# Kernel optimization log

Hardware: AMD Instinct MI355X
Metric: run time of the kernel (lower is better)

## Reference

```python
import jax, jax.numpy as jnp
import numpy as np

HEAD_DIM = 256
N_Q = 8
N_KV = 4
HIDDEN = 2304
WINDOW = 1024
SOFT_CAP = 50.0
MAX_WAVELENGTH = 10000.0


def _rope(x, start_index=0):
    # x: [b, s, n, h]. keras_hub RotaryEmbedding (rotate-half convention),
    # followed by Gemma's interleave permutation of the feature dim.
    b, s, n, h = x.shape
    inv_freq = 1.0 / (MAX_WAVELENGTH ** (jnp.arange(0, h, 2, dtype=jnp.float32) / h))
    pos = jnp.arange(s, dtype=jnp.float32) + start_index
    freq = pos[:, None] * inv_freq[None, :]            # [s, h/2]
    emb = jnp.concatenate([freq, freq], axis=-1)[None, :, None, :]  # [1, s, 1, h]
    cos, sin = jnp.cos(emb).astype(x.dtype), jnp.sin(emb).astype(x.dtype)
    x1, x2 = jnp.split(x, 2, axis=-1)
    rot = jnp.concatenate([-x2, x1], axis=-1)
    y = x * cos + rot * sin
    # Gemma _apply_rope: split halves then interleave (same permutation on q and k)
    a, b2 = jnp.split(y, 2, axis=-1)
    return jnp.stack([a, b2], axis=-1).reshape(x.shape)


def setup_inputs() -> dict:
    key = jax.random.key(0)
    ks = jax.random.split(key, 5)
    B, T, D = 2, 2048, HIDDEN
    x = jax.random.normal(ks[0], (B, T, D), dtype=jnp.float32)
    # causal mask [b, q_len, kv_len]
    causal = jnp.tril(jnp.ones((T, T), dtype=bool))
    attention_mask = jnp.broadcast_to(causal[None], (B, T, T))
    scale = 0.02
    Wq = jax.random.normal(ks[1], (N_Q, D, HEAD_DIM), dtype=jnp.float32) * scale
    Wk = jax.random.normal(ks[2], (N_KV, D, HEAD_DIM), dtype=jnp.float32) * scale
    Wv = jax.random.normal(ks[3], (N_KV, D, HEAD_DIM), dtype=jnp.float32) * scale
    Wo = jax.random.normal(ks[4], (N_Q, HEAD_DIM, D), dtype=jnp.float32) * scale
    return {"x": x, "attention_mask": attention_mask, "Wq": Wq, "Wk": Wk, "Wv": Wv, "Wo": Wo}


def reference(x, attention_mask, Wq, Wk, Wv, Wo):
    b, t, d = x.shape
    q = jnp.einsum('btd,ndh->btnh', x, Wq)
    k = jnp.einsum('bsd,kdh->bskh', x, Wk)
    v = jnp.einsum('bsd,kdh->bskh', x, Wv)
    q = _rope(q)
    k = _rope(k)
    s = k.shape[1]
    # sliding window band mask (triu(-w+1) & tril(w-1)), rows sliced at cache_update_index=0
    i = jnp.arange(s)[:, None]
    j = jnp.arange(s)[None, :]
    sliding = (j - i <= WINDOW - 1) & (i - j <= WINDOW - 1)
    mask = attention_mask & sliding[None, :t, :s]      # [b, t, s]
    q = q * jnp.asarray(1.0 / np.sqrt(HEAD_DIM), dtype=q.dtype)
    g = N_Q // N_KV
    qg = q.reshape(b, t, N_KV, g, HEAD_DIM)
    logits = jnp.einsum('btkgh,bskh->bkgts', qg, k).astype(jnp.float32)
    logits = jnp.tanh(logits / SOFT_CAP) * SOFT_CAP    # logit soft-cap
    m = mask[:, None, None, :, :]                      # [b, 1, 1, t, s]
    logits = jnp.where(m, logits, jnp.float32(-1e30))
    probs = jax.nn.softmax(logits, axis=-1).astype(q.dtype)
    out = jnp.einsum('bkgts,bskh->btkgh', probs, v).reshape(b, t, N_Q, HEAD_DIM)
    no_attended = jnp.all(~attention_mask, axis=-1, keepdims=True)[..., None]  # [b, t, 1, 1]
    out = jnp.where(no_attended, jnp.zeros_like(out), out)
    return jnp.einsum('btnh,nhd->btd', out, Wo)
```

## Files before the change

kernel.cpp:

```cpp
#include <hip/hip_runtime.h>
#include <math.h>

#define HEAD_DIM 256
#define N_Q 8
#define N_KV 4
#define HIDDEN 2304
#define WINDOW 1024
#define BATCH 2
#define SEQ 2048
#define BT (BATCH*SEQ)

typedef unsigned short u16;
typedef __attribute__((ext_vector_type(8))) short bf16x8;
typedef __attribute__((ext_vector_type(4))) float f32x4;

__device__ __forceinline__ u16 f2bf(float f) {
    union { float f; unsigned u; } c; c.f = f;
    unsigned r = c.u + 0x7FFF + ((c.u >> 16) & 1);
    return (u16)(r >> 16);
}
__device__ __forceinline__ float bf2f(u16 b) {
    union { float f; unsigned u; } c; c.u = ((unsigned)b) << 16;
    return c.f;
}

__global__ __launch_bounds__(256) void convert_x_kernel(
    const float* __restrict__ x, u16* __restrict__ xb, int n8)
{
    int i = blockIdx.x * 256 + threadIdx.x;
    if (i >= n8) return;
    const float4 a = ((const float4*)x)[2*i];
    const float4 b = ((const float4*)x)[2*i+1];
    u16 o[8] = { f2bf(a.x), f2bf(a.y), f2bf(a.z), f2bf(a.w),
                 f2bf(b.x), f2bf(b.y), f2bf(b.z), f2bf(b.w) };
    ((uint4*)xb)[i] = *(const uint4*)o;
}

__global__ __launch_bounds__(256) void wqkv_t_kernel(
    const float* __restrict__ Wq, const float* __restrict__ Wk,
    const float* __restrict__ Wv, u16* __restrict__ Wt)
{
    __shared__ float t[64][65];
    const int j = blockIdx.z;
    const float* W = (j < 8)  ? Wq + (size_t)j*HIDDEN*HEAD_DIM
                   : (j < 12) ? Wk + (size_t)(j-8)*HIDDEN*HEAD_DIM
                              : Wv + (size_t)(j-12)*HIDDEN*HEAD_DIM;
    const int d0 = blockIdx.x * 64, h0 = blockIdx.y * 64;
    const int tid = threadIdx.x;
    {
        const int r = tid >> 4, c4 = tid & 15;
        #pragma unroll
        for (int rr = r; rr < 64; rr += 16) {
            const float4 v = *(const float4*)(W + (size_t)(d0+rr)*HEAD_DIM + h0 + c4*4);
            t[rr][c4*4+0] = v.x; t[rr][c4*4+1] = v.y;
            t[rr][c4*4+2] = v.z; t[rr][c4*4+3] = v.w;
        }
    }
    __syncthreads();
    {
        const int hh = tid >> 2;
        #pragma unroll
        for (int it = 0; it < 2; it++) {
            const int chunk = (tid & 3) + it*4;
            u16 tmp[8];
            #pragma unroll
            for (int jj = 0; jj < 8; jj++) tmp[jj] = f2bf(t[chunk*8+jj][hh]);
            *(uint4*)&Wt[(size_t)(j*256 + h0 + hh)*HIDDEN + d0 + chunk*8] = *(const uint4*)tmp;
        }
    }
}

__global__ __launch_bounds__(256) void wo_t_kernel(
    const float* __restrict__ Wo, u16* __restrict__ Wot)
{
    __shared__ float t[64][65];
    const int k0 = blockIdx.x * 64, d0 = blockIdx.y * 64;
    const int tid = threadIdx.x;
    {
        const int r = tid >> 4, c4 = tid & 15;
        #pragma unroll
        for (int rr = r; rr < 64; rr += 16) {
            const float4 v = *(const float4*)(Wo + (size_t)(k0+rr)*HIDDEN + d0 + c4*4);
            t[rr][c4*4+0] = v.x; t[rr][c4*4+1] = v.y;
            t[rr][c4*4+2] = v.z; t[rr][c4*4+3] = v.w;
        }
    }
    __syncthreads();
    {
        const int dd = tid >> 2;
        #pragma unroll
        for (int it = 0; it < 2; it++) {
            const int chunk = (tid & 3) + it*4;
            u16 tmp[8];
            #pragma unroll
            for (int jj = 0; jj < 8; jj++) tmp[jj] = f2bf(t[chunk*8+jj][dd]);
            *(uint4*)&Wot[(size_t)(d0 + dd)*(N_Q*HEAD_DIM) + k0 + chunk*8] = *(const uint4*)tmp;
        }
    }
}

template<int KK>
__device__ __forceinline__ void g256_ld_b(const u16 (&BsB)[16384], bf16x8 (&bf)[4],
                                          int wcol, int l16, int quad, int axor)
{
    #pragma unroll
    for (int j = 0; j < 4; j++)
        bf[j] = *(const bf16x8*)(&BsB[(wcol*64 + j*16 + l16)*64 + (((KK<<2)|quad)^axor)*8]);
}
template<int MH, int KK>
__device__ __forceinline__ void g256_ld_a(const u16 (&AsB)[16384], bf16x8 (&af)[4],
                                          int wrow, int l16, int quad, int axor)
{
    #pragma unroll
    for (int i = 0; i < 4; i++)
        af[i] = *(const bf16x8*)(&AsB[(wrow*128 + MH*64 + i*16 + l16)*64 + (((KK<<2)|quad)^axor)*8]);
}
template<int MH>
__device__ __forceinline__ void g256_mfma(const bf16x8 (&af)[4], const bf16x8 (&bf)[4],
                                          f32x4 (&acc)[8][4])
{
    __builtin_amdgcn_s_setprio(1);
    #pragma unroll
    for (int i = 0; i < 4; i++)
        #pragma unroll
        for (int j = 0; j < 4; j++)
            acc[MH*4+i][j] = __builtin_amdgcn_mfma_f32_16x16x32_bf16(
                                 af[i], bf[j], acc[MH*4+i][j], 0, 0, 0);
    __builtin_amdgcn_s_setprio(0);
}

#define STG256(DST, SRCP, R0, KT)                                              \
    __builtin_amdgcn_global_load_lds(                                          \
        (const __attribute__((address_space(1))) unsigned int*)                \
            ((SRCP) + (size_t)(R0)*K + (size_t)(KT)*64),                       \
        (__attribute__((address_space(3))) unsigned int*)                      \
            (&DST[((R0) + wave*8)*64]),                                        \
        16, 0, 0)

#define WAITV(N) asm volatile("s_waitcnt vmcnt(" #N ")" ::: "memory")
#define BAR()    __builtin_amdgcn_s_barrier()

template<typename OutT>
__global__ __launch_bounds__(512, 2) void gemm256_kernel(
    const u16* __restrict__ A, const u16* __restrict__ Bt,
    OutT* __restrict__ C, int M, int N, int K)
{
    __shared__ __align__(16) u16 As0[16384];
    __shared__ __align__(16) u16 As1[16384];
    __shared__ __align__(16) u16 Bs0[16384];
    __shared__ __align__(16) u16 Bs1[16384];

    const int nwg = gridDim.x;
    const int bid = blockIdx.x;
    const int cpx = nwg >> 3;
    const int swz = (bid & 7) * cpx + (bid >> 3);
    const int NX  = N >> 8;
    const int m0  = (swz / NX) << 8;
    const int n0  = (swz % NX) << 8;

    const int tid  = threadIdx.x;
    const int lane = tid & 63;
    const int wave = tid >> 6;
    const int wrow = wave >> 2;
    const int wcol = wave & 3;
    const int l16  = lane & 15;
    const int quad = lane >> 4;
    const int axor = l16 & 7;

    const int srow8  = lane >> 3;
    const int schunk = (lane & 7) ^ srow8;
    const u16* Ag = A  + (size_t)(m0 + wave*8 + srow8)*K + schunk*8;
    const u16* Bg = Bt + (size_t)(n0 + wave*8 + srow8)*K + schunk*8;

    f32x4 acc[8][4];
    #pragma unroll
    for (int i = 0; i < 8; i++)
        #pragma unroll
        for (int j = 0; j < 4; j++) acc[i][j] = (f32x4){0.f,0.f,0.f,0.f};
    bf16x8 af[4], bf[4];

    STG256(Bs0, Bg,   0, 0); STG256(Bs0, Bg,  64, 0);
    STG256(Bs0, Bg, 128, 0); STG256(Bs0, Bg, 192, 0);
    STG256(As0, Ag,   0, 0); STG256(As0, Ag, 128, 0);
    STG256(As0, Ag,  64, 0); STG256(As0, Ag, 192, 0);
    STG256(Bs1, Bg,   0, 1); STG256(Bs1, Bg,  64, 1);
    WAITV(4);
    BAR();

    const int NT2 = K >> 7;
    for (int t = 0; t < NT2; ++t) {
        const int T1 = 2*t+1, T2 = 2*t+2, T3 = 2*t+3;
        const bool nl = (t < NT2-1);

        g256_ld_b<0>(Bs0, bf, wcol, l16, quad, axor);
        g256_ld_a<0,0>(As0, af, wrow, l16, quad, axor);
        STG256(Bs1, Bg, 128, T1); STG256(Bs1, Bg, 192, T1);
        BAR();
        g256_mfma<0>(af, bf, acc);
        WAITV(4);
        BAR();

        g256_ld_a<1,0>(As0, af, wrow, l16, quad, axor);
        STG256(As1, Ag, 0, T1); STG256(As1, Ag, 128, T1);
        BAR();
        g256_mfma<1>(af, bf, acc);
        BAR();

        g256_ld_b<1>(Bs0, bf, wcol, l16, quad, axor);
        g256_ld_a<0,1>(As0, af, wrow, l16, quad, axor);
        STG256(As1, Ag, 64, T1); STG256(As1, Ag, 192, T1);
        BAR();
        g256_mfma<0>(af, bf, acc);
        BAR();

        g256_ld_a<1,1>(As0, af, wrow, l16, quad, axor);
        if (nl) { STG256(Bs0, Bg, 0, T2); STG256(Bs0, Bg, 64, T2); }
        BAR();
        g256_mfma<1>(af, bf, acc);
        if (nl) { WAITV(4); }
        else    { WAITV(0); }
        BAR();

        g256_ld_b<0>(Bs1, bf, wcol, l16, quad, axor);
        g256_ld_a<0,0>(As1, af, wrow, l16, quad, axor);
        if (nl) { STG256(Bs0, Bg, 128, T2); STG256(Bs0, Bg, 192, T2); }
        BAR();
        g256_mfma<0>(af, bf, acc);
        WAITV(4);
        BAR();

        g256_ld_a<1,0>(As1, af, wrow, l16, quad, axor);
        if (nl) { STG256(As0, Ag, 0, T2); STG256(As0, Ag, 128, T2); }
        BAR();
        g256_mfma<1>(af, bf, acc);
        BAR();

        g256_ld_b<1>(Bs1, bf, wcol, l16, quad, axor);
        g256_ld_a<0,1>(As1, af, wrow, l16, quad, axor);
        if (nl) { STG256(As0, Ag, 64, T2); STG256(As0, Ag, 192, T2); }
        BAR();
        g256_mfma<0>(af, bf, acc);
        BAR();

        g256_ld_a<1,1>(As1, af, wrow, l16, quad, axor);
        if (nl) { STG256(Bs1, Bg, 0, T3); STG256(Bs1, Bg, 64, T3); }
        BAR();
        g256_mfma<1>(af, bf, acc);
        WAITV(4);
        BAR();
    }

    #pragma unroll
    for (int ii = 0; ii < 8; ii++) {
        const int rbase = m0 + wrow*128 + ii*16 + quad*4;
        #pragma unroll
        for (int j = 0; j < 4; j++) {
            const int col = n0 + wcol*64 + j*16 + l16;
            #pragma unroll
            for (int r = 0; r < 4; r++) {
                const float v = acc[ii][j][r];
                if constexpr (sizeof(OutT) == 2)
                    ((u16*)C)[(size_t)(rbase + r)*N + col] = f2bf(v);
                else
                    ((float*)C)[(size_t)(rbase + r)*N + col] = v;
            }
        }
    }
}

__global__ __launch_bounds__(256) void rope_kernel(
    const u16* __restrict__ raw, u16* __restrict__ qb, u16* __restrict__ kbf)
{
    const int r   = blockIdx.x;
    const int pos = r & (SEQ-1);
    const int tid = threadIdx.x;
    const u16* row = raw + (size_t)r * 4096;
    const float LOG1E4 = 9.210340371976184f;

    #pragma unroll
    for (int p = tid; p < 1024; p += 256) {
        const int n = p >> 7, j = p & 127;
        const float lo = bf2f(row[n*256 + j]);
        const float hi = bf2f(row[n*256 + j + 128]);
        const float inv = __expf(-LOG1E4 * (float)j * (1.0f/128.0f));
        float s, c; sincosf((float)pos * inv, &s, &c);
        qb[((size_t)r*N_Q + n)*HEAD_DIM + j]       = f2bf((lo*c - hi*s) * 0.0625f);
        qb[((size_t)r*N_Q + n)*HEAD_DIM + j + 128] = f2bf((hi*c + lo*s) * 0.0625f);
    }
    #pragma unroll
    for (int p = tid; p < 512; p += 256) {
        const int n = p >> 7, j = p & 127;
        const float lo = bf2f(row[2048 + n*256 + j]);
        const float hi = bf2f(row[2048 + n*256 + j + 128]);
        const float inv = __expf(-LOG1E4 * (float)j * (1.0f/128.0f));
        float s, c; sincosf((float)pos * inv, &s, &c);
        kbf[((size_t)r*N_KV + n)*HEAD_DIM + j]       = f2bf(lo*c - hi*s);
        kbf[((size_t)r*N_KV + n)*HEAD_DIM + j + 128] = f2bf(hi*c + lo*s);
    }
}

__global__ __launch_bounds__(256) void vtrans_kernel(
    const u16* __restrict__ raw, u16* __restrict__ vtt)
{
    __shared__ u16 T[32*264];
    const int blk = blockIdx.x;
    const int sc  = blk & 63;
    const int bk  = blk >> 6;
    const int b   = bk >> 2, kh = bk & 3;
    const int tid = threadIdx.x;

    const u16* rrow = raw + (size_t)(b*SEQ + sc*32)*4096 + 3072 + kh*256;
    {
        const int s = tid >> 3;
        #pragma unroll
        for (int it = 0; it < 4; it++) {
            const int seg = (tid & 7) + it*8;
            *(uint4*)&T[s*264 + seg*8] = *(const uint4*)(rrow + (size_t)s*4096 + seg*8);
        }
    }
    __syncthreads();
    u16* out = vtt + (size_t)blk*8192;
    #pragma unroll
    for (int it = 0; it < 4; it++) {
        const int o = tid + it*256;
        const int h = o >> 2, ss = o & 3;
        u16 tmp[8];
        #pragma unroll
        for (int j = 0; j < 8; j++) tmp[j] = T[(ss*8 + j)*264 + h];
        *(uint4*)(out + h*32 + ((ss ^ (h & 3))*8)) = *(const uint4*)tmp;
    }
}

#define AQT 64
__global__ __launch_bounds__(256) void attn_mfma_kernel(
    const u16* __restrict__ qb, const u16* __restrict__ kb,
    const u16* __restrict__ vtt, u16* __restrict__ ao)
{
    __shared__ u16 Ks[32*264];
    __shared__ u16 Vs[256*32];
    __shared__ u16 Ps[64*40];
    __shared__ float lsum[64];

    const int qh = blockIdx.y;
    const int kh = qh >> 1;
    const int bx = ((blockIdx.y >> 2) & 1) ? (gridDim.x - 1 - (int)blockIdx.x)
                                           : (int)blockIdx.x;
    const int t0 = bx * AQT;
    const int b  = t0 >> 11;
    const int tb = t0 & (SEQ-1);
    const int tid  = threadIdx.x;
    const int wave = tid >> 6;
    const int lane = tid & 63;
    const int l16  = lane & 15;
    const int quad = lane >> 4;

    bf16x8 qf[8];
    {
        const u16* qrow = qb + ((size_t)(t0 + wave*16 + l16)*N_Q + qh)*HEAD_DIM + quad*8;
        #pragma unroll
        for (int c = 0; c < 8; c++) qf[c] = *(const bf16x8*)(qrow + c*32);
    }

    f32x4 o[4][4];
    #pragma unroll
    for (int i = 0; i < 4; i++)
        #pragma unroll
        for (int j = 0; j < 4; j++) o[i][j] = (f32x4){0.f,0.f,0.f,0.f};
    float lpart[4] = {0.f, 0.f, 0.f, 0.f};

    int s_begin = tb - (WINDOW-1); if (s_begin < 0) s_begin = 0;
    const int st0 = s_begin & ~31;

    const u16* kbase = kb  + ((size_t)(b*SEQ)*N_KV + kh)*HEAD_DIM;
    const u16* vbase = vtt + ((size_t)(b*N_KV + kh)*SEQ)*HEAD_DIM;

    for (int st = st0; st < tb + AQT; st += 32) {
        __syncthreads();
        {
            const u16* vtile = vbase + (size_t)st*HEAD_DIM;
            #pragma unroll
            for (int c = 0; c < 4; c++) {
                const int off = wave*2048 + c*512;
                __builtin_amdgcn_global_load_lds(
                    (const __attribute__((address_space(1))) unsigned int*)(vtile + off + lane*8),
                    (__attribute__((address_space(3))) unsigned int*)&Vs[off],
                    16, 0, 0);
            }
            const int s = tid >> 3;
            const u16* krow = kbase + (size_t)(st + s)*(N_KV*HEAD_DIM);
            #pragma unroll
            for (int it = 0; it < 4; it++) {
                const int seg = (tid & 7) + it*8;
                *(uint4*)&Ks[s*264 + seg*8] = *(const uint4*)(krow + seg*8);
            }
        }
        __syncthreads();

        f32x4 sc[2];
        #pragma unroll
        for (int sf = 0; sf < 2; sf++) {
            f32x4 a = (f32x4){0.f,0.f,0.f,0.f};
            const u16* kr = &Ks[(sf*16 + l16)*264 + quad*8];
            #pragma unroll
            for (int c = 0; c < 8; c++)
                a = __builtin_amdgcn_mfma_f32_16x16x32_bf16(
                        qf[c], *(const bf16x8*)(kr + c*32), a, 0, 0, 0);
            sc[sf] = a;
        }

        #pragma unroll
        for (int sf = 0; sf < 2; sf++) {
            const int sg = st + sf*16 + l16;
            #pragma unroll
            for (int r = 0; r < 4; r++) {
                const int tg = tb + wave*16 + quad*4 + r;
                const float e1 = __expf(sc[sf][r] * 0.04f);
                float p = __expf(-100.0f / (e1 + 1.0f));
                const bool ok = (sg <= tg) && (tg - sg < WINDOW);
                p = ok ? p : 0.0f;
                lpart[r] += p;
                Ps[(wave*16 + quad*4 + r)*40 + sf*16 + l16] = f2bf(p);
            }
        }
        __syncthreads();

        bf16x8 ap[4];
        #pragma unroll
        for (int i = 0; i < 4; i++)
            ap[i] = *(const bf16x8*)&Ps[(i*16 + l16)*40 + quad*8];
        #pragma unroll
        for (int j = 0; j < 4; j++) {
            const int hr = wave*64 + j*16 + l16;
            const bf16x8 bv = *(const bf16x8*)&Vs[hr*32 + ((quad ^ (l16 & 3))*8)];
            #pragma unroll
            for (int i = 0; i < 4; i++)
                o[i][j] = __builtin_amdgcn_mfma_f32_16x16x32_bf16(ap[i], bv, o[i][j], 0, 0, 0);
        }
    }

    #pragma unroll
    for (int r = 0; r < 4; r++) {
        float s = lpart[r];
        #pragma unroll
        for (int sh = 1; sh <= 8; sh <<= 1) s += __shfl_xor(s, sh, 64);
        if (l16 == 0) lsum[wave*16 + quad*4 + r] = s;
    }
    __syncthreads();

    #pragma unroll
    for (int i = 0; i < 4; i++) {
        #pragma unroll
        for (int r = 0; r < 4; r++) {
            const int rl  = i*16 + quad*4 + r;
            const float inv = 1.0f / (lsum[rl] + 1e-30f);
            u16* arow = ao + ((size_t)(t0 + rl)*N_Q + qh)*HEAD_DIM + wave*64 + l16;
            #pragma unroll
            for (int j = 0; j < 4; j++)
                arow[j*16] = f2bf(o[i][j][r] * inv);
        }
    }
}

extern "C" void kernel_launch(void* const* d_in, const int* in_sizes, int n_in,
                              void* d_out, int out_size, void* d_ws, size_t ws_size,
                              hipStream_t stream)
{
    const float* x  = (const float*)d_in[0];
    const float* Wq = (const float*)d_in[2];
    const float* Wk = (const float*)d_in[3];
    const float* Wv = (const float*)d_in[4];
    const float* Wo = (const float*)d_in[5];
    float* out = (float*)d_out;

    char* w = (char*)d_ws;
    u16* qbuf = (u16*)(w);
    u16* kbuf = (u16*)(w +  16777216ull);
    u16* vtt  = (u16*)(w +  25165824ull);
    u16* aob  = (u16*)(w +  33554432ull);
    u16* xb   = (u16*)(w +  50331648ull);
    u16* wt1  = (u16*)(w +  69206016ull);
    u16* wot  = (u16*)(w +  88080384ull);
    u16* raw  = (u16*)(w +  97517568ull);

    const int n8 = BT*HIDDEN/8;
    convert_x_kernel<<<(n8+255)/256, 256, 0, stream>>>(x, xb, n8);
    wqkv_t_kernel<<<dim3(HIDDEN/64, HEAD_DIM/64, 16), 256, 0, stream>>>(Wq, Wk, Wv, wt1);
    wo_t_kernel<<<dim3(N_Q*HEAD_DIM/64, HIDDEN/64), 256, 0, stream>>>(Wo, wot);

    gemm256_kernel<u16><<<(BT/256)*(4096/256), 512, 0, stream>>>(
        xb, wt1, raw, BT, 4096, HIDDEN);
    rope_kernel<<<BT, 256, 0, stream>>>(raw, qbuf, kbuf);
    vtrans_kernel<<<BATCH*N_KV*64, 256, 0, stream>>>(raw, vtt);
    attn_mfma_kernel<<<dim3(BT/AQT, N_Q), 256, 0, stream>>>(qbuf, kbuf, vtt, aob);
    gemm256_kernel<float><<<(BT/256)*(HIDDEN/256), 512, 0, stream>>>(
        aob, wot, out, BT, HIDDEN, N_Q*HEAD_DIM);
}
```

Before: 372.7 us.

## Restructure GEMM to 4-stage BK=32 LDS pipeline with double-buffered fragments

Reworks the 256x256 GEMM main loop from two BK=64 LDS buffers to four BK=32 stages, with a matching swizzle and a new global-to-LDS load mapping. It double-buffers the A and B register fragments (X/Y) so fragment reads for the next MFMA group overlap the current one, and adds sched_barriers to pin the ordering. The aim is deeper prefetch and better hiding of load latency under the MFMAs. In exchange it executes more barriers per unit of K, and fragment double-buffering raises register pressure under launch_bounds(512,2).

Result: slower. 386.3 us (+3.7%).

```diff
diff --git a/kernel.cpp b/kernel.cpp
--- a/kernel.cpp
+++ b/kernel.cpp
@@ -99,25 +99,23 @@
     }
 }
 
-template<int KK>
-__device__ __forceinline__ void g256_ld_b(const u16 (&BsB)[16384], bf16x8 (&bf)[4],
-                                          int wcol, int l16, int quad, int axor)
+__device__ __forceinline__ void ldA4(const u16 (&B)[8192], bf16x8 (&s)[4],
+                                     int base, int MH)
+{
+    #pragma unroll
+    for (int i = 0; i < 4; i++)
+        s[i] = *(const bf16x8*)&B[base + MH*2048 + i*512];
+}
+__device__ __forceinline__ void ldB4(const u16 (&B)[8192], bf16x8 (&s)[4],
+                                     int base)
 {
     #pragma unroll
     for (int j = 0; j < 4; j++)
-        bf[j] = *(const bf16x8*)(&BsB[(wcol*64 + j*16 + l16)*64 + (((KK<<2)|quad)^axor)*8]);
-}
-template<int MH, int KK>
-__device__ __forceinline__ void g256_ld_a(const u16 (&AsB)[16384], bf16x8 (&af)[4],
-                                          int wrow, int l16, int quad, int axor)
-{
-    #pragma unroll
-    for (int i = 0; i < 4; i++)
-        af[i] = *(const bf16x8*)(&AsB[(wrow*128 + MH*64 + i*16 + l16)*64 + (((KK<<2)|quad)^axor)*8]);
+        s[j] = *(const bf16x8*)&B[base + j*512];
 }
 template<int MH>
-__device__ __forceinline__ void g256_mfma(const bf16x8 (&af)[4], const bf16x8 (&bf)[4],
-                                          f32x4 (&acc)[8][4])
+__device__ __forceinline__ void mfma16(const bf16x8 (&af)[4], const bf16x8 (&bf)[4],
+                                       f32x4 (&acc)[8][4])
 {
     __builtin_amdgcn_s_setprio(1);
     #pragma unroll
@@ -129,26 +127,32 @@
     __builtin_amdgcn_s_setprio(0);
 }
 
-#define STG256(DST, SRCP, R0, KT)                                              \
+#define WAITV(N) asm volatile("s_waitcnt vmcnt(" #N ")" ::: "memory")
+#define BAR()    __builtin_amdgcn_s_barrier()
+#define SCHEDB() __builtin_amdgcn_sched_barrier(0)
+
+#define STG(DST, SRCP, R0, KT)                                                 \
     __builtin_amdgcn_global_load_lds(                                          \
         (const __attribute__((address_space(1))) unsigned int*)                \
-            ((SRCP) + (size_t)(R0)*K + (size_t)(KT)*64),                       \
+            ((SRCP) + (size_t)(R0)*K + (size_t)(KT)*32),                       \
         (__attribute__((address_space(3))) unsigned int*)                      \
-            (&DST[((R0) + wave*8)*64]),                                        \
+            (&DST[((R0) + wave*16)*32]),                                       \
         16, 0, 0)
-
-#define WAITV(N) asm volatile("s_waitcnt vmcnt(" #N ")" ::: "memory")
-#define BAR()    __builtin_amdgcn_s_barrier()
+#define STG2(DST, SRCP, KT) do { STG(DST, SRCP, 0, KT); STG(DST, SRCP, 128, KT); } while(0)
 
 template<typename OutT>
 __global__ __launch_bounds__(512, 2) void gemm256_kernel(
     const u16* __restrict__ A, const u16* __restrict__ Bt,
     OutT* __restrict__ C, int M, int N, int K)
 {
-    __shared__ __align__(16) u16 As0[16384];
-    __shared__ __align__(16) u16 As1[16384];
-    __shared__ __align__(16) u16 Bs0[16384];
-    __shared__ __align__(16) u16 Bs1[16384];
+    __shared__ __align__(16) u16 As0[8192];
+    __shared__ __align__(16) u16 As1[8192];
+    __shared__ __align__(16) u16 As2[8192];
+    __shared__ __align__(16) u16 As3[8192];
+    __shared__ __align__(16) u16 Bs0[8192];
+    __shared__ __align__(16) u16 Bs1[8192];
+    __shared__ __align__(16) u16 Bs2[8192];
+    __shared__ __align__(16) u16 Bs3[8192];
 
     const int nwg = gridDim.x;
     const int bid = blockIdx.x;
@@ -165,89 +169,116 @@
     const int wcol = wave & 3;
     const int l16  = lane & 15;
     const int quad = lane >> 4;
-    const int axor = l16 & 7;
-
-    const int srow8  = lane >> 3;
-    const int schunk = (lane & 7) ^ srow8;
-    const u16* Ag = A  + (size_t)(m0 + wave*8 + srow8)*K + schunk*8;
-    const u16* Bg = Bt + (size_t)(n0 + wave*8 + srow8)*K + schunk*8;
+
+    const int srow4  = lane >> 2;
+    const int schunk = (lane & 3) ^ (srow4 & 3);
+    const u16* Ag = A  + (size_t)(m0 + wave*16 + srow4)*K + schunk*8;
+    const u16* Bg = Bt + (size_t)(n0 + wave*16 + srow4)*K + schunk*8;
+
+    const int quad2 = quad ^ (l16 & 3);
+    const int aBase = (wrow*128 + l16)*32 + quad2*8;
+    const int bBase = (wcol*64  + l16)*32 + quad2*8;
 
     f32x4 acc[8][4];
     #pragma unroll
     for (int i = 0; i < 8; i++)
         #pragma unroll
         for (int j = 0; j < 4; j++) acc[i][j] = (f32x4){0.f,0.f,0.f,0.f};
-    bf16x8 af[4], bf[4];
-
-    STG256(Bs0, Bg,   0, 0); STG256(Bs0, Bg,  64, 0);
-    STG256(Bs0, Bg, 128, 0); STG256(Bs0, Bg, 192, 0);
-    STG256(As0, Ag,   0, 0); STG256(As0, Ag, 128, 0);
-    STG256(As0, Ag,  64, 0); STG256(As0, Ag, 192, 0);
-    STG256(Bs1, Bg,   0, 1); STG256(Bs1, Bg,  64, 1);
-    WAITV(4);
+    bf16x8 afX[4], afY[4], bfX[4], bfY[4];
+
+    STG2(Bs0, Bg, 0); STG2(As0, Ag, 0);
+    STG2(Bs1, Bg, 1); STG2(As1, Ag, 1);
+    STG2(Bs2, Bg, 2); STG2(As2, Ag, 2);
+    WAITV(8);
     BAR();
-
-    const int NT2 = K >> 7;
-    for (int t = 0; t < NT2; ++t) {
-        const int T1 = 2*t+1, T2 = 2*t+2, T3 = 2*t+3;
-        const bool nl = (t < NT2-1);
-
-        g256_ld_b<0>(Bs0, bf, wcol, l16, quad, axor);
-        g256_ld_a<0,0>(As0, af, wrow, l16, quad, axor);
-        STG256(Bs1, Bg, 128, T1); STG256(Bs1, Bg, 192, T1);
-        BAR();
-        g256_mfma<0>(af, bf, acc);
-        WAITV(4);
-        BAR();
-
-        g256_ld_a<1,0>(As0, af, wrow, l16, quad, axor);
-        STG256(As1, Ag, 0, T1); STG256(As1, Ag, 128, T1);
-        BAR();
-        g256_mfma<1>(af, bf, acc);
-        BAR();
-
-        g256_ld_b<1>(Bs0, bf, wcol, l16, quad, axor);
-        g256_ld_a<0,1>(As0, af, wrow, l16, quad, axor);
-        STG256(As1, Ag, 64, T1); STG256(As1, Ag, 192, T1);
-        BAR();
-        g256_mfma<0>(af, bf, acc);
-        BAR();
-
-        g256_ld_a<1,1>(As0, af, wrow, l16, quad, axor);
-        if (nl) { STG256(Bs0, Bg, 0, T2); STG256(Bs0, Bg, 64, T2); }
-        BAR();
-        g256_mfma<1>(af, bf, acc);
-        if (nl) { WAITV(4); }
-        else    { WAITV(0); }
-        BAR();
-
-        g256_ld_b<0>(Bs1, bf, wcol, l16, quad, axor);
-        g256_ld_a<0,0>(As1, af, wrow, l16, quad, axor);
-        if (nl) { STG256(Bs0, Bg, 128, T2); STG256(Bs0, Bg, 192, T2); }
-        BAR();
-        g256_mfma<0>(af, bf, acc);
-        WAITV(4);
-        BAR();
-
-        g256_ld_a<1,0>(As1, af, wrow, l16, quad, axor);
-        if (nl) { STG256(As0, Ag, 0, T2); STG256(As0, Ag, 128, T2); }
-        BAR();
-        g256_mfma<1>(af, bf, acc);
-        BAR();
-
-        g256_ld_b<1>(Bs1, bf, wcol, l16, quad, axor);
-        g256_ld_a<0,1>(As1, af, wrow, l16, quad, axor);
-        if (nl) { STG256(As0, Ag, 64, T2); STG256(As0, Ag, 192, T2); }
-        BAR();
-        g256_mfma<0>(af, bf, acc);
-        BAR();
-
-        g256_ld_a<1,1>(As1, af, wrow, l16, quad, axor);
-        if (nl) { STG256(Bs1, Bg, 0, T3); STG256(Bs1, Bg, 64, T3); }
-        BAR();
-        g256_mfma<1>(af, bf, acc);
-        WAITV(4);
-        BAR();
+    ldB4(Bs0, bfX, bBase);
+    ldA4(As0, afX, aBase, 0);
+
+    const int NT = K >> 5;
+
+    for (int t = 0; t < NT-4; t += 4) {
+        ldA4(As0, afY, aBase, 1);
+        STG2(Bs3, Bg, t+3);
+        WAITV(6); SCHEDB(); BAR();
+        mfma16<0>(afX, bfX, acc);
+        BAR();
+        ldB4(Bs1, bfY, bBase);
+        ldA4(As1, afX, aBase, 0);
+        STG2(As3, Ag, t+3);
+        SCHEDB(); BAR();
+        mfma16<1>(afY, bfX, acc);
+        BAR();
+        ldA4(As1, afY, aBase, 1);
+        STG2(Bs0, Bg, t+4);
+        WAITV(6); SCHEDB(); BAR();
+        mfma16<0>(afX, bfY, acc);
+        BAR();
+        ldB4(Bs2, bfX, bBase);
+        ldA4(As2, afX, aBase, 0);
+        STG2(As0, Ag, t+4);
+        SCHEDB(); BAR();
+        mfma16<1>(afY, bfY, acc);
+        BAR();
+        ldA4(As2, afY, aBase, 1);
+        STG2(Bs1, Bg, t+5);
+        WAITV(6); SCHEDB(); BAR();
+        mfma16<0>(afX, bfX, acc);
+        BAR();
+        ldB4(Bs3, bfY, bBase);
+        ldA4(As3, afX, aBase, 0);
+        STG2(As1, Ag, t+5);
+        SCHEDB(); BAR();
+        mfma16<1>(afY, bfX, acc);
+        BAR();
+        ldA4(As3, afY, aBase, 1);
+        STG2(Bs2, Bg, t+6);
+        WAITV(6); SCHEDB(); BAR();
+        mfma16<0>(afX, bfY, acc);
+        BAR();
+        ldB4(Bs0, bfX, bBase);
+        ldA4(As0, afX, aBase, 0);
+        STG2(As2, Ag, t+6);
+        SCHEDB(); BAR();
+        mfma16<1>(afY, bfY, acc);
+        BAR();
+    }
+
+    {
+        const int t = NT-4;
+        ldA4(As0, afY, aBase, 1);
+        STG2(Bs3, Bg, t+3);
+        WAITV(6); SCHEDB(); BAR();
+        mfma16<0>(afX, bfX, acc);
+        BAR();
+        ldB4(Bs1, bfY, bBase);
+        ldA4(As1, afX, aBase, 0);
+        STG2(As3, Ag, t+3);
+        SCHEDB(); BAR();
+        mfma16<1>(afY, bfX, acc);
+        BAR();
+        ldA4(As1, afY, aBase, 1);
+        WAITV(4); SCHEDB(); BAR();
+        mfma16<0>(afX, bfY, acc);
+        BAR();
+        ldB4(Bs2, bfX, bBase);
+        ldA4(As2, afX, aBase, 0);
+        SCHEDB(); BAR();
+        mfma16<1>(afY, bfY, acc);
+        BAR();
+        ldA4(As2, afY, aBase, 1);
+        WAITV(0); SCHEDB(); BAR();
+        mfma16<0>(afX, bfX, acc);
+        BAR();
+        ldB4(Bs3, bfY, bBase);
+        ldA4(As3, afX, aBase, 0);
+        SCHEDB(); BAR();
+        mfma16<1>(afY, bfX, acc);
+        BAR();
+        ldA4(As3, afY, aBase, 1);
+        SCHEDB(); BAR();
+        mfma16<0>(afX, bfY, acc);
+        BAR();
+        mfma16<1>(afY, bfY, acc);
     }
 
     #pragma unroll
@@ -267,6 +298,9 @@
         }
     }
 }
+
+#undef STG2
+#undef STG
 
 __global__ __launch_bounds__(256) void rope_kernel(
     const u16* __restrict__ raw, u16* __restrict__ qb, u16* __restrict__ kbf)
```

## Double-buffer GEMM fragment registers to overlap LDS reads with MFMA

Applied to the files above, without the earlier changes.

Splits the A/B fragment registers into two sets (X/Y) so the LDS read for the next sub-step is issued before the MFMA batch of the current one, giving a one-stage software pipeline with a peeled prologue and epilogue. Adds sched_barrier fences and loosens the vmcnt waits so global-to-LDS loads stay in flight longer. The aim is to hide LDS read latency behind matrix work. In exchange it uses more VGPRs under the 512-thread, 2-block launch bound, which may cause spills, and it relies on subtle correctness of barrier and wait placement.

After: 386.1 us. 3.6% more time.

```diff
diff --git a/kernel.cpp b/kernel.cpp
--- a/kernel.cpp
+++ b/kernel.cpp
@@ -139,6 +139,7 @@
 
 #define WAITV(N) asm volatile("s_waitcnt vmcnt(" #N ")" ::: "memory")
 #define BAR()    __builtin_amdgcn_s_barrier()
+#define SCHEDB() __builtin_amdgcn_sched_barrier(0)
 
 template<typename OutT>
 __global__ __launch_bounds__(512, 2) void gemm256_kernel(
@@ -177,77 +178,119 @@
     for (int i = 0; i < 8; i++)
         #pragma unroll
         for (int j = 0; j < 4; j++) acc[i][j] = (f32x4){0.f,0.f,0.f,0.f};
-    bf16x8 af[4], bf[4];
+    bf16x8 afX[4], afY[4], bfX[4], bfY[4];
 
     STG256(Bs0, Bg,   0, 0); STG256(Bs0, Bg,  64, 0);
     STG256(Bs0, Bg, 128, 0); STG256(Bs0, Bg, 192, 0);
     STG256(As0, Ag,   0, 0); STG256(As0, Ag, 128, 0);
     STG256(As0, Ag,  64, 0); STG256(As0, Ag, 192, 0);
     STG256(Bs1, Bg,   0, 1); STG256(Bs1, Bg,  64, 1);
-    WAITV(4);
+    WAITV(2);
     BAR();
+    g256_ld_b<0>(Bs0, bfX, wcol, l16, quad, axor);
+    g256_ld_a<0,0>(As0, afX, wrow, l16, quad, axor);
 
     const int NT2 = K >> 7;
-    for (int t = 0; t < NT2; ++t) {
+
+    for (int t = 0; t < NT2-1; ++t) {
         const int T1 = 2*t+1, T2 = 2*t+2, T3 = 2*t+3;
-        const bool nl = (t < NT2-1);
-
-        g256_ld_b<0>(Bs0, bf, wcol, l16, quad, axor);
-        g256_ld_a<0,0>(As0, af, wrow, l16, quad, axor);
+
+        g256_ld_a<1,0>(As0, afY, wrow, l16, quad, axor);
         STG256(Bs1, Bg, 128, T1); STG256(Bs1, Bg, 192, T1);
-        BAR();
-        g256_mfma<0>(af, bf, acc);
-        WAITV(4);
-        BAR();
-
-        g256_ld_a<1,0>(As0, af, wrow, l16, quad, axor);
+        SCHEDB(); BAR();
+        g256_mfma<0>(afX, bfX, acc);
+        BAR();
+
+        g256_ld_b<1>(Bs0, bfY, wcol, l16, quad, axor);
+        g256_ld_a<0,1>(As0, afX, wrow, l16, quad, axor);
         STG256(As1, Ag, 0, T1); STG256(As1, Ag, 128, T1);
-        BAR();
-        g256_mfma<1>(af, bf, acc);
-        BAR();
-
-        g256_ld_b<1>(Bs0, bf, wcol, l16, quad, axor);
-        g256_ld_a<0,1>(As0, af, wrow, l16, quad, axor);
+        SCHEDB(); BAR();
+        g256_mfma<1>(afY, bfX, acc);
+        BAR();
+
+        g256_ld_a<1,1>(As0, afY, wrow, l16, quad, axor);
         STG256(As1, Ag, 64, T1); STG256(As1, Ag, 192, T1);
-        BAR();
-        g256_mfma<0>(af, bf, acc);
-        BAR();
-
-        g256_ld_a<1,1>(As0, af, wrow, l16, quad, axor);
-        if (nl) { STG256(Bs0, Bg, 0, T2); STG256(Bs0, Bg, 64, T2); }
-        BAR();
-        g256_mfma<1>(af, bf, acc);
-        if (nl) { WAITV(4); }
-        else    { WAITV(0); }
-        BAR();
-
-        g256_ld_b<0>(Bs1, bf, wcol, l16, quad, axor);
-        g256_ld_a<0,0>(As1, af, wrow, l16, quad, axor);
-        if (nl) { STG256(Bs0, Bg, 128, T2); STG256(Bs0, Bg, 192, T2); }
-        BAR();
-        g256_mfma<0>(af, bf, acc);
-        WAITV(4);
-        BAR();
-
-        g256_ld_a<1,0>(As1, af, wrow, l16, quad, axor);
-        if (nl) { STG256(As0, Ag, 0, T2); STG256(As0, Ag, 128, T2); }
-        BAR();
-        g256_mfma<1>(af, bf, acc);
-        BAR();
-
-        g256_ld_b<1>(Bs1, bf, wcol, l16, quad, axor);
-        g256_ld_a<0,1>(As1, af, wrow, l16, quad, axor);
-        if (nl) { STG256(As0, Ag, 64, T2); STG256(As0, Ag, 192, T2); }
-        BAR();
-        g256_mfma<0>(af, bf, acc);
-        BAR();
-
-        g256_ld_a<1,1>(As1, af, wrow, l16, quad, axor);
-        if (nl) { STG256(Bs1, Bg, 0, T3); STG256(Bs1, Bg, 64, T3); }
-        BAR();
-        g256_mfma<1>(af, bf, acc);
-        WAITV(4);
-        BAR();
+        SCHEDB(); BAR();
+        g256_mfma<0>(afX, bfY, acc);
+        WAITV(2);
+        BAR();
+
+        g256_ld_b<0>(Bs1, bfX, wcol, l16, quad, axor);
+        g256_ld_a<0,0>(As1, afX, wrow, l16, quad, axor);
+        STG256(Bs0, Bg, 0, T2); STG256(Bs0, Bg, 64, T2);
+        SCHEDB(); BAR();
+        g256_mfma<1>(afY, bfY, acc);
+        WAITV(2);
+        BAR();
+
+        g256_ld_a<1,0>(As1, afY, wrow, l16, quad, axor);
+        STG256(Bs0, Bg, 128, T2); STG256(Bs0, Bg, 192, T2);
+        SCHEDB(); BAR();
+        g256_mfma<0>(afX, bfX, acc);
+        BAR();
+
+        g256_ld_b<1>(Bs1, bfY, wcol, l16, quad, axor);
+        g256_ld_a<0,1>(As1, afX, wrow, l16, quad, axor);
+        STG256(As0, Ag, 0, T2); STG256(As0, Ag, 128, T2);
+        SCHEDB(); BAR();
+        g256_mfma<1>(afY, bfX, acc);
+        BAR();
+
+        g256_ld_a<1,1>(As1, afY, wrow, l16, quad, axor);
+        STG256(As0, Ag, 64, T2); STG256(As0, Ag, 192, T2);
+        SCHEDB(); BAR();
+        g256_mfma<0>(afX, bfY, acc);
+        WAITV(2);
+        BAR();
+
+        g256_ld_b<0>(Bs0, bfX, wcol, l16, quad, axor);
+        g256_ld_a<0,0>(As0, afX, wrow, l16, quad, axor);
+        STG256(Bs1, Bg, 0, T3); STG256(Bs1, Bg, 64, T3);
+        SCHEDB(); BAR();
+        g256_mfma<1>(afY, bfY, acc);
+        WAITV(2);
+        BAR();
+    }
+
+    {
+        const int T1 = 2*(NT2-1)+1;
+        g256_ld_a<1,0>(As0, afY, wrow, l16, quad, axor);
+        STG256(Bs1, Bg, 128, T1); STG256(Bs1, Bg, 192, T1);
+        SCHEDB(); BAR();
+        g256_mfma<0>(afX, bfX, acc);
+        BAR();
+        g256_ld_b<1>(Bs0, bfY, wcol, l16, quad, axor);
+        g256_ld_a<0,1>(As0, afX, wrow, l16, quad, axor);
+        STG256(As1, Ag, 0, T1); STG256(As1, Ag, 128, T1);
+        SCHEDB(); BAR();
+        g256_mfma<1>(afY, bfX, acc);
+        BAR();
+        g256_ld_a<1,1>(As0, afY, wrow, l16, quad, axor);
+        STG256(As1, Ag, 64, T1); STG256(As1, Ag, 192, T1);
+        SCHEDB(); BAR();
+        g256_mfma<0>(afX, bfY, acc);
+        WAITV(2);
+        BAR();
+        g256_ld_b<0>(Bs1, bfX, wcol, l16, quad, axor);
+        g256_ld_a<0,0>(As1, afX, wrow, l16, quad, axor);
+        SCHEDB(); BAR();
+        g256_mfma<1>(afY, bfY, acc);
+        WAITV(0);
+        BAR();
+        g256_ld_a<1,0>(As1, afY, wrow, l16, quad, axor);
+        SCHEDB(); BAR();
+        g256_mfma<0>(afX, bfX, acc);
+        BAR();
+        g256_ld_b<1>(Bs1, bfY, wcol, l16, quad, axor);
+        g256_ld_a<0,1>(As1, afX, wrow, l16, quad, axor);
+        SCHEDB(); BAR();
+        g256_mfma<1>(afY, bfX, acc);
+        BAR();
+        g256_ld_a<1,1>(As1, afY, wrow, l16, quad, axor);
+        SCHEDB(); BAR();
+        g256_mfma<0>(afX, bfY, acc);
+        BAR();
+        g256_mfma<1>(afY, bfY, acc);
     }
 
     #pragma unroll
@@ -267,6 +310,8 @@
         }
     }
 }
+
+#undef STG256
 
 __global__ __launch_bounds__(256) void rope_kernel(
     const u16* __restrict__ raw, u16* __restrict__ qb, u16* __restrict__ kbf)
```
